# Performance work log

Hardware: AMD Instinct MI355X
Metric: run time of the kernel (lower is better)

## Reference

```python
import jax, jax.numpy as jnp
import numpy as np

B, T, I, H, L = 32, 1024, 1024, 1024, 3


def setup_inputs() -> dict:
    key = jax.random.key(0)
    ks = jax.random.split(key, 8)
    sc_in = 1.0 / np.sqrt(I)
    sc_h = 1.0 / np.sqrt(H)
    return {
        "x": jax.random.normal(ks[0], (B, T, I), dtype=jnp.float32),
        "s0": jnp.zeros((B, H), dtype=jnp.float32),
        "w_h": jax.random.normal(ks[1], (I, H), dtype=jnp.float32) * sc_in,
        "w_t": jax.random.normal(ks[2], (I, H), dtype=jnp.float32) * sc_in,
        "w_c": jax.random.normal(ks[3], (I, H), dtype=jnp.float32) * sc_in,
        "Rh": jax.random.normal(ks[4], (L, H, H), dtype=jnp.float32) * sc_h,
        "Rt": jax.random.normal(ks[5], (L, H, H), dtype=jnp.float32) * sc_h,
        "Rc": jax.random.normal(ks[6], (L, H, H), dtype=jnp.float32) * sc_h,
        "bh": jnp.zeros((L, H), dtype=jnp.float32),
        "bt": jnp.zeros((L, H), dtype=jnp.float32),
        "bc": jnp.zeros((L, H), dtype=jnp.float32),
    }


def reference(x, s0, w_h, w_t, w_c, Rh, Rt, Rc, bh, bt, bc):
    # x: [B, T, I]; s0: [B, H]. Dropout prob = 0 -> identity.
    num_layers = Rh.shape[0]

    def step(s, x_t):
        # Input projections only feed layer 0 (as in the torch code).
        whx = x_t @ w_h  # [B, H]
        wtx = x_t @ w_t
        wcx = x_t @ w_c
        for l in range(num_layers):
            h_in = (whx if l == 0 else 0.0) + s @ Rh[l].T + bh[l]
            t_in = (wtx if l == 0 else 0.0) + s @ Rt[l].T + bt[l]
            c_in = (wcx if l == 0 else 0.0) + s @ Rc[l].T + bc[l]
            h = jnp.tanh(h_in)
            t = jax.nn.sigmoid(t_in)
            c = jax.nn.sigmoid(c_in)
            s = h * t + s * c
        return s, s

    x_tbi = jnp.swapaxes(x, 0, 1)  # [T, B, I] for scan over time
    s_T, outs = jax.lax.scan(step, s0, x_tbi)
    return jnp.swapaxes(outs, 0, 1), s_T  # ([B, T, H], [B, H])
```

## Files before the change

### kernel.cpp

```cpp
#include <hip/hip_runtime.h>
#include <hip/hip_bf16.h>

static constexpr int Bb = 32;
static constexpr int Tt = 1024;
static constexpr int Ii = 1024;
static constexpr int Hh = 1024;
static constexpr int NWG = 256;

static constexpr int HSLOT = Hh * 16;
static constexpr int NSLOT2 = 2 * (3 * Tt + 1);

typedef float f4 __attribute__((ext_vector_type(4)));

static constexpr int LDS_WORDS = 36 * 1024 + 4 * 12 * 16;
static constexpr int LDS_BYTES = LDS_WORDS * 4;

static constexpr int SYNC_BYTES = 4096;

template <typename PT> __device__ __forceinline__ float pt_to_f(PT v);
template <> __device__ __forceinline__ float pt_to_f<float>(float v) { return v; }
template <> __device__ __forceinline__ float pt_to_f<__hip_bfloat16>(__hip_bfloat16 v) { return __bfloat162float(v); }

template <typename PT> __device__ __forceinline__ PT f_to_pt(float v);
template <> __device__ __forceinline__ float f_to_pt<float>(float v) { return v; }
template <> __device__ __forceinline__ __hip_bfloat16 f_to_pt<__hip_bfloat16>(float v) { return __float2bfloat16(v); }

#define CGLD(dst, p, lit) \
    asm volatile("global_load_dwordx4 %0, %1, off offset:" lit : "=v"(dst) : "v"(p))
#define GB4(sv, p, a,b,c,d2) \
    CGLD(sv[0],p,a); CGLD(sv[1],p,b); CGLD(sv[2],p,c); CGLD(sv[3],p,d2)
#define VWAIT(n) do { asm volatile("s_waitcnt vmcnt(" #n ")" ::: "memory"); \
                      __builtin_amdgcn_sched_barrier(0); } while (0)

template <typename PT>
__global__ __launch_bounds__(256, 2) void proj_gemm(
    const float* __restrict__ X, const float* __restrict__ Wh,
    const float* __restrict__ Wt, const float* __restrict__ Wc,
    PT* __restrict__ P2)
{
    __shared__ float smem[4160];
    float* As = smem;
    float* Bs = smem + 1088;

    const int tid = threadIdx.x;
    const int tx = tid & 15, ty = tid >> 4;
    const int col0 = blockIdx.x * 64;
    const int t0 = blockIdx.y * 2;

    float acc[3][4][4];
#pragma unroll
    for (int g = 0; g < 3; ++g)
#pragma unroll
        for (int mm = 0; mm < 4; ++mm)
#pragma unroll
            for (int nn = 0; nn < 4; ++nn) acc[g][mm][nn] = 0.f;

    const int lm = tid >> 2, lk4 = (tid & 3) * 4;
    const float* aptr = X + ((size_t)(lm & 31) * Tt + (t0 + (lm >> 5))) * Ii + lk4;
    const int bk = tid >> 4, bn4 = (tid & 15) * 4;

    for (int k0 = 0; k0 < Ii; k0 += 16) {
        float4 av = *(const float4*)(aptr + k0);
        As[(lk4 + 0) * 68 + lm] = av.x;
        As[(lk4 + 1) * 68 + lm] = av.y;
        As[(lk4 + 2) * 68 + lm] = av.z;
        As[(lk4 + 3) * 68 + lm] = av.w;
        *(float4*)&Bs[0 * 1024 + bk * 64 + bn4] = *(const float4*)(Wh + (size_t)(k0 + bk) * Hh + col0 + bn4);
        *(float4*)&Bs[1 * 1024 + bk * 64 + bn4] = *(const float4*)(Wt + (size_t)(k0 + bk) * Hh + col0 + bn4);
        *(float4*)&Bs[2 * 1024 + bk * 64 + bn4] = *(const float4*)(Wc + (size_t)(k0 + bk) * Hh + col0 + bn4);
        __syncthreads();
#pragma unroll
        for (int k = 0; k < 16; ++k) {
            float4 a = *(const float4*)&As[k * 68 + ty * 4];
            float a_[4] = {a.x, a.y, a.z, a.w};
#pragma unroll
            for (int g = 0; g < 3; ++g) {
                float4 b = *(const float4*)&Bs[g * 1024 + k * 64 + tx * 4];
                float b_[4] = {b.x, b.y, b.z, b.w};
#pragma unroll
                for (int mm = 0; mm < 4; ++mm)
#pragma unroll
                    for (int nn = 0; nn < 4; ++nn)
                        acc[g][mm][nn] += a_[mm] * b_[nn];
            }
        }
        __syncthreads();
    }

    float* E = smem;
    const int b4 = (tid & 7) * 4;
#pragma unroll 1
    for (int g = 0; g < 3; ++g) {
        __syncthreads();
#pragma unroll
        for (int mm = 0; mm < 4; ++mm)
#pragma unroll
            for (int nn = 0; nn < 4; ++nn)
                E[(ty * 4 + mm) * 65 + tx * 4 + nn] = acc[g][mm][nn];
        __syncthreads();
        PT* dst = P2 + (size_t)g * Tt * Hh * Bb;
#pragma unroll
        for (int it = 0; it < 4; ++it) {
            const int line = (tid >> 3) + it * 32;
            const int tt = line >> 6, hh = line & 63;
            const float o0 = E[(tt * 32 + b4 + 0) * 65 + hh];
            const float o1 = E[(tt * 32 + b4 + 1) * 65 + hh];
            const float o2v = E[(tt * 32 + b4 + 2) * 65 + hh];
            const float o3 = E[(tt * 32 + b4 + 3) * 65 + hh];
            PT* d = dst + ((size_t)(t0 + tt) * Hh + col0 + hh) * Bb + b4;
            d[0] = f_to_pt<PT>(o0); d[1] = f_to_pt<PT>(o1);
            d[2] = f_to_pt<PT>(o2v); d[3] = f_to_pt<PT>(o3);
        }
    }
}

template <typename RT>
__global__ void init_k(const float* __restrict__ s0, RT* __restrict__ ring)
{
    const int i = blockIdx.x * 256 + threadIdx.x;
    if (i < Bb * Hh) {
        const int b = i >> 10, h = i & 1023;
        const int grp = b >> 4, bl = b & 15;
        ring[(size_t)grp * HSLOT + h * 16 + bl] = f_to_pt<RT>(s0[i]);
    }
}

template <typename RT>
__global__ __launch_bounds__(256) void out_transpose(
    const RT* __restrict__ ring, float* __restrict__ out, float* __restrict__ sT)
{
    __shared__ float tile[128 * 33];
    const int tid = threadIdx.x;
    const int h0 = blockIdx.x * 128;
    const int t = blockIdx.y;
    const RT* srcA = ring + (size_t)((3 * t + 3) * 2) * HSLOT + h0 * 16;
    const RT* srcB = srcA + HSLOT;
#pragma unroll
    for (int e = 0; e < 16; ++e) {
        const int idx = e * 256 + tid;
        const int h = idx >> 5, b = idx & 31;
        const float v = (b < 16) ? pt_to_f<RT>(srcA[h * 16 + b])
                                 : pt_to_f<RT>(srcB[h * 16 + (b - 16)]);
        tile[h * 33 + b] = v;
    }
    __syncthreads();
    const int hi = tid & 31, bq = tid >> 5;
#pragma unroll
    for (int e = 0; e < 4; ++e) {
        const int b = bq + e * 8;
        float4 v;
        v.x = tile[(hi * 4 + 0) * 33 + b];
        v.y = tile[(hi * 4 + 1) * 33 + b];
        v.z = tile[(hi * 4 + 2) * 33 + b];
        v.w = tile[(hi * 4 + 3) * 33 + b];
        *(float4*)(out + ((size_t)b * Tt + t) * Hh + h0 + hi * 4) = v;
        if (t == Tt - 1) *(float4*)(sT + (size_t)b * Hh + h0 + hi * 4) = v;
    }
}

__device__ __forceinline__ void poll256(unsigned* flags, int tid, unsigned ph)
{
    if (tid < 64) {
        for (;;) {
            const unsigned v0 = __hip_atomic_load(&flags[tid],       __ATOMIC_RELAXED, __HIP_MEMORY_SCOPE_AGENT);
            const unsigned v1 = __hip_atomic_load(&flags[tid + 64],  __ATOMIC_RELAXED, __HIP_MEMORY_SCOPE_AGENT);
            const unsigned v2 = __hip_atomic_load(&flags[tid + 128], __ATOMIC_RELAXED, __HIP_MEMORY_SCOPE_AGENT);
            const unsigned v3 = __hip_atomic_load(&flags[tid + 192], __ATOMIC_RELAXED, __HIP_MEMORY_SCOPE_AGENT);
            if (__all((int)((v0 >= ph) & (v1 >= ph) & (v2 >= ph) & (v3 >= ph)))) break;
            __builtin_amdgcn_s_sleep(2);
        }
    }
    __syncthreads();
}

template <typename PT, typename RT>
__global__ __launch_bounds__(256, 1) void rhn_recur(
    const float* __restrict__ Rh, const float* __restrict__ Rt,
    const float* __restrict__ Rc, const float* __restrict__ bh,
    const float* __restrict__ bt, const float* __restrict__ bc,
    const PT* __restrict__ P2, RT* __restrict__ ring,
    unsigned* __restrict__ flagsA, unsigned* __restrict__ flagsB)
{
    extern __shared__ float lds[];
    float* part = lds + 36 * 1024;

    const int g = blockIdx.x;
    const int tid = threadIdx.x;

    {
        const int k4 = tid * 4;
        const int sk = k4 ^ (((k4 >> 5) & 3) << 2);
#pragma unroll 1
        for (int j = 0; j < 36; ++j) {
            const int l = j / 12;
            const int rem = j - l * 12;
            const int gt = rem >> 2;
            const int q = rem & 3;
            const int h = (q << 8) | g;
            const float* src = (gt == 0 ? Rh : (gt == 1 ? Rt : Rc)) + ((size_t)l * Hh + h) * Hh;
            *(float4*)&lds[(j << 10) | sk] = *(const float4*)(src + k4);
        }
    }
    __syncthreads();

    const int ks = tid >> 2;
    const int bq = tid & 3;
    const int b0 = bq << 2;
    const int wv = tid >> 6;
    const int jsel = ks & 15;
    const int ubb = tid & 15;
    const int uq  = (tid >> 4) & 3;
    const int uhc = (uq << 8) | g;

    int o2[4];
#pragma unroll
    for (int c = 0; c < 4; ++c)
        o2[c] = (((ks << 4) | (c << 2))) ^ ((((ks << 4) >> 5) & 3) << 2);

    float brh[3], brt[3], brc[3];
#pragma unroll
    for (int l = 0; l < 3; ++l) {
        brh[l] = bh[l * Hh + uhc];
        brt[l] = bt[l * Hh + uhc];
        brc[l] = bc[l * Hh + uhc];
    }

    float soA = pt_to_f<RT>(ring[uhc * 16 + ubb]);
    float soB = pt_to_f<RT>(ring[(size_t)HSLOT + uhc * 16 + ubb]);

    const size_t THB = (size_t)Tt * Hh * Bb;
    float pvA0 = 0.f, pvA1 = 0.f, pvA2 = 0.f, pvB0 = 0.f, pvB1 = 0.f, pvB2 = 0.f;
    auto loadP = [&](int tt) {
        if (tid < 64) {
            const size_t pb = ((size_t)tt * Hh + uhc) * Bb + ubb;
            pvA0 = pt_to_f<PT>(P2[pb]);
            pvA1 = pt_to_f<PT>(P2[THB + pb]);
            pvA2 = pt_to_f<PT>(P2[2 * THB + pb]);
            pvB0 = pt_to_f<PT>(P2[pb + 16]);
            pvB1 = pt_to_f<PT>(P2[THB + pb + 16]);
            pvB2 = pt_to_f<PT>(P2[2 * THB + pb + 16]);
        }
    };
    loadP(0);

    auto halfstep = [&](const float* rp, const RT* rs, RT* rw, float& so,
                        float pv0, float pv1, float pv2, bool addP,
                        float bb0, float bb1, float bb2) {
        f4 accv[12];
#pragma unroll
        for (int jj = 0; jj < 12; ++jj) accv[jj] = (f4){0.f, 0.f, 0.f, 0.f};

        if constexpr (sizeof(RT) == 4) {
            const float* sA = (const float*)rs + (size_t)(ks << 4) * 16 + b0;
            f4 sv0[4], sv1[4], sv2[4], sv3[4];
            GB4(sv0, sA, "0","64","128","192");
            GB4(sv1, sA, "256","320","384","448");
            GB4(sv2, sA, "512","576","640","704");
            GB4(sv3, sA, "768","832","896","960");
            VWAIT(12);
#pragma unroll
            for (int jj = 0; jj < 12; ++jj) {
                const f4 r = *(const f4*)(rp + jj * 1024 + o2[0]);
                f4 a = accv[jj];
                a += sv0[0] * r[0]; a += sv0[1] * r[1]; a += sv0[2] * r[2]; a += sv0[3] * r[3];
                accv[jj] = a;
            }
            VWAIT(8);
#pragma unroll
            for (int jj = 0; jj < 12; ++jj) {
                const f4 r = *(const f4*)(rp + jj * 1024 + o2[1]);
                f4 a = accv[jj];
                a += sv1[0] * r[0]; a += sv1[1] * r[1]; a += sv1[2] * r[2]; a += sv1[3] * r[3];
                accv[jj] = a;
            }
            VWAIT(4);
#pragma unroll
            for (int jj = 0; jj < 12; ++jj) {
                const f4 r = *(const f4*)(rp + jj * 1024 + o2[2]);
                f4 a = accv[jj];
                a += sv2[0] * r[0]; a += sv2[1] * r[1]; a += sv2[2] * r[2]; a += sv2[3] * r[3];
                accv[jj] = a;
            }
            VWAIT(0);
#pragma unroll
            for (int jj = 0; jj < 12; ++jj) {
                const f4 r = *(const f4*)(rp + jj * 1024 + o2[3]);
                f4 a = accv[jj];
                a += sv3[0] * r[0]; a += sv3[1] * r[1]; a += sv3[2] * r[2]; a += sv3[3] * r[3];
                accv[jj] = a;
            }
        } else {
            const __hip_bfloat16* sIn = (const __hip_bfloat16*)rs + (size_t)(ks << 4) * 16 + b0;
#pragma unroll
            for (int blk = 0; blk < 4; ++blk) {
                f4 sv[4];
#pragma unroll
                for (int i = 0; i < 4; ++i) {
                    const ushort4 u = *(const ushort4*)(sIn + (size_t)(blk * 4 + i) * 16);
                    sv[i][0] = __uint_as_float((unsigned)u.x << 16);
                    sv[i][1] = __uint_as_float((unsigned)u.y << 16);
                    sv[i][2] = __uint_as_float((unsigned)u.z << 16);
                    sv[i][3] = __uint_as_float((unsigned)u.w << 16);
                }
#pragma unroll
                for (int jj = 0; jj < 12; ++jj) {
                    const f4 r = *(const f4*)(rp + jj * 1024 + o2[blk]);
                    f4 a = accv[jj];
                    a += sv[0] * r[0]; a += sv[1] * r[1]; a += sv[2] * r[2]; a += sv[3] * r[3];
                    accv[jj] = a;
                }
            }
        }

#pragma unroll
        for (int jj = 0; jj < 12; ++jj) {
#pragma unroll
            for (int st = 4; st <= 32; st <<= 1) {
                accv[jj][0] += __shfl_xor(accv[jj][0], st);
                accv[jj][1] += __shfl_xor(accv[jj][1], st);
                accv[jj][2] += __shfl_xor(accv[jj][2], st);
                accv[jj][3] += __shfl_xor(accv[jj][3], st);
            }
        }
        f4 s1 = accv[0];
#pragma unroll
        for (int j2 = 1; j2 < 12; ++j2) if (jsel == j2) s1 = accv[j2];
        if (jsel < 12) *(f4*)&part[wv * 192 + jsel * 16 + b0] = s1;
        __syncthreads();

        if (tid < 64) {
            float vals[3];
#pragma unroll
            for (int gt = 0; gt < 3; ++gt) {
                const int jl = (gt << 2) + uq;
                vals[gt] = part[jl * 16 + ubb] + part[192 + jl * 16 + ubb]
                         + part[384 + jl * 16 + ubb] + part[576 + jl * 16 + ubb];
            }
            vals[0] += bb0; vals[1] += bb1; vals[2] += bb2;
            if (addP) { vals[0] += pv0; vals[1] += pv1; vals[2] += pv2; }
            const float hv = 1.f - 2.f / (1.f + __expf(2.f * vals[0]));
            const float tv = 1.f / (1.f + __expf(-vals[1]));
            const float cv = 1.f / (1.f + __expf(-vals[2]));
            const float sn = hv * tv + so * cv;
            so = sn;
            RT* wp = rw + uhc * 16 + ubb;
            if constexpr (sizeof(RT) == 4) {
                __hip_atomic_store((float*)wp, sn, __ATOMIC_RELAXED, __HIP_MEMORY_SCOPE_AGENT);
            } else {
                __hip_bfloat16 b16 = __float2bfloat16(sn);
                __hip_atomic_store((unsigned short*)wp, *(unsigned short*)&b16,
                                   __ATOMIC_RELAXED, __HIP_MEMORY_SCOPE_AGENT);
            }
        }
        __syncthreads();
    };

#pragma unroll 1
    for (int t = 0; t < Tt; ++t) {
#pragma unroll 1
        for (int l = 0; l < 3; ++l) {
            const int p = t * 3 + l;
            float bb0, bb1, bb2;
            if (l == 0)      { bb0 = brh[0]; bb1 = brt[0]; bb2 = brc[0]; }
            else if (l == 1) { bb0 = brh[1]; bb1 = brt[1]; bb2 = brc[1]; }
            else             { bb0 = brh[2]; bb1 = brt[2]; bb2 = brc[2]; }
            const float* rp = lds + l * 12288;

            poll256(flagsA, tid, (unsigned)p);
            halfstep(rp, ring + (size_t)(p * 2 + 0) * HSLOT,
                         ring + (size_t)((p + 1) * 2 + 0) * HSLOT,
                     soA, pvA0, pvA1, pvA2, l == 0, bb0, bb1, bb2);
            if (tid == 0)
                __hip_atomic_store(&flagsA[g], (unsigned)(p + 1), __ATOMIC_RELAXED, __HIP_MEMORY_SCOPE_AGENT);

            poll256(flagsB, tid, (unsigned)p);
            halfstep(rp, ring + (size_t)(p * 2 + 1) * HSLOT,
                         ring + (size_t)((p + 1) * 2 + 1) * HSLOT,
                     soB, pvB0, pvB1, pvB2, l == 0, bb0, bb1, bb2);
            if (tid == 0)
                __hip_atomic_store(&flagsB[g], (unsigned)(p + 1), __ATOMIC_RELAXED, __HIP_MEMORY_SCOPE_AGENT);

            if (l == 2 && t + 1 < Tt) loadP(t + 1);
        }
    }
}

extern "C" void kernel_launch(void* const* d_in, const int* in_sizes, int n_in,
                              void* d_out, int out_size, void* d_ws, size_t ws_size,
                              hipStream_t stream)
{
    (void)in_sizes; (void)n_in; (void)out_size;
    const float* x  = (const float*)d_in[0];
    const float* s0 = (const float*)d_in[1];
    const float* wh = (const float*)d_in[2];
    const float* wt = (const float*)d_in[3];
    const float* wc = (const float*)d_in[4];
    const float* Rh = (const float*)d_in[5];
    const float* Rt = (const float*)d_in[6];
    const float* Rc = (const float*)d_in[7];
    const float* bh = (const float*)d_in[8];
    const float* bt = (const float*)d_in[9];
    const float* bc = (const float*)d_in[10];

    float* out = (float*)d_out;
    float* sT  = out + (size_t)Bb * Tt * Hh;

    const size_t THB  = (size_t)Tt * Hh * Bb;
    const size_t p2f  = 3 * THB * 4, p2h = 3 * THB * 2;
    const size_t ringF = (size_t)NSLOT2 * HSLOT * 4;
    const size_t ringH = (size_t)NSLOT2 * HSLOT * 2;

    char* w = (char*)d_ws;

    if (ws_size >= p2f + ringF + SYNC_BYTES) {
        float* P2 = (float*)w;
        float* ring = (float*)(w + p2f);
        unsigned* flagsA = (unsigned*)(w + p2f + ringF);
        unsigned* flagsB = flagsA + 256;
        hipMemsetAsync(flagsA, 0, SYNC_BYTES, stream);
        proj_gemm<float><<<dim3(16, 512), 256, 0, stream>>>(x, wh, wt, wc, P2);
        init_k<float><<<128, 256, 0, stream>>>(s0, ring);
        hipFuncSetAttribute(reinterpret_cast<const void*>(rhn_recur<float, float>),
                            hipFuncAttributeMaxDynamicSharedMemorySize, LDS_BYTES);
        void* args[] = {(void*)&Rh, (void*)&Rt, (void*)&Rc, (void*)&bh, (void*)&bt, (void*)&bc,
                        (void*)&P2, (void*)&ring, (void*)&flagsA, (void*)&flagsB};
        hipLaunchCooperativeKernel(reinterpret_cast<void*>(rhn_recur<float, float>),
                                   dim3(NWG), dim3(256), args, LDS_BYTES, stream);
        out_transpose<float><<<dim3(8, 1024), 256, 0, stream>>>(ring, out, sT);
    } else if (ws_size >= p2h + ringF + SYNC_BYTES) {
        __hip_bfloat16* P2 = (__hip_bfloat16*)w;
        float* ring = (float*)(w + p2h);
        unsigned* flagsA = (unsigned*)(w + p2h + ringF);
        unsigned* flagsB = flagsA + 256;
        hipMemsetAsync(flagsA, 0, SYNC_BYTES, stream);
        proj_gemm<__hip_bfloat16><<<dim3(16, 512), 256, 0, stream>>>(x, wh, wt, wc, P2);
        init_k<float><<<128, 256, 0, stream>>>(s0, ring);
        hipFuncSetAttribute(reinterpret_cast<const void*>(rhn_recur<__hip_bfloat16, float>),
                            hipFuncAttributeMaxDynamicSharedMemorySize, LDS_BYTES);
        void* args[] = {(void*)&Rh, (void*)&Rt, (void*)&Rc, (void*)&bh, (void*)&bt, (void*)&bc,
                        (void*)&P2, (void*)&ring, (void*)&flagsA, (void*)&flagsB};
        hipLaunchCooperativeKernel(reinterpret_cast<void*>(rhn_recur<__hip_bfloat16, float>),
                                   dim3(NWG), dim3(256), args, LDS_BYTES, stream);
        out_transpose<float><<<dim3(8, 1024), 256, 0, stream>>>(ring, out, sT);
    } else {
        __hip_bfloat16* P2 = (__hip_bfloat16*)w;
        __hip_bfloat16* ring = (__hip_bfloat16*)(w + p2h);
        unsigned* flagsA = (unsigned*)(w + p2h + ringH);
        unsigned* flagsB = flagsA + 256;
        hipMemsetAsync(flagsA, 0, SYNC_BYTES, stream);
        proj_gemm<__hip_bfloat16><<<dim3(16, 512), 256, 0, stream>>>(x, wh, wt, wc, P2);
        init_k<__hip_bfloat16><<<128, 256, 0, stream>>>(s0, ring);
        hipFuncSetAttribute(reinterpret_cast<const void*>(rhn_recur<__hip_bfloat16, __hip_bfloat16>),
                            hipFuncAttributeMaxDynamicSharedMemorySize, LDS_BYTES);
        void* args[] = {(void*)&Rh, (void*)&Rt, (void*)&Rc, (void*)&bh, (void*)&bt, (void*)&bc,
                        (void*)&P2, (void*)&ring, (void*)&flagsA, (void*)&flagsB};
        hipLaunchCooperativeKernel(reinterpret_cast<void*>(rhn_recur<__hip_bfloat16, __hip_bfloat16>),
                                   dim3(NWG), dim3(256), args, LDS_BYTES, stream);
        out_transpose<__hip_bfloat16><<<dim3(8, 1024), 256, 0, stream>>>(ring, out, sT);
    }
}
```

Measured before the change: 33.34 ms.

## Replace flag-based grid barriers with sentinel-poisoned ring data polling

Removes the per-half-step flag arrays and all-workgroup polling barriers. The state ring is pre-filled with a NaN sentinel pattern, and consumers spin on the actual data loads (retrying with cache-bypassing loads) until no sentinel values remain. The per-halfstep syncthreads goes away by double-buffering the LDS partial-sum area, and the next-timestep P prefetch is moved earlier. This trades a full grid-wide barrier for fine-grained dataflow waiting, at the cost of a larger init kernel that writes the whole ring and reliance on stores becoming visible atomically per element.

```diff
diff --git a/kernel.cpp b/kernel.cpp
--- a/kernel.cpp
+++ b/kernel.cpp
@@ -12,10 +12,11 @@
 
 typedef float f4 __attribute__((ext_vector_type(4)));
 
-static constexpr int LDS_WORDS = 36 * 1024 + 4 * 12 * 16;
+static constexpr int LDS_WORDS = 36 * 1024 + 2 * 768;
 static constexpr int LDS_BYTES = LDS_WORDS * 4;
 
-static constexpr int SYNC_BYTES = 4096;
+static constexpr unsigned SENT32 = 0x7FC0DEADu;
+static constexpr unsigned SENT16 = 0x7FC1u;
 
 template <typename PT> __device__ __forceinline__ float pt_to_f(PT v);
 template <> __device__ __forceinline__ float pt_to_f<float>(float v) { return v; }
@@ -27,10 +28,48 @@
 
 #define CGLD(dst, p, lit) \
     asm volatile("global_load_dwordx4 %0, %1, off offset:" lit : "=v"(dst) : "v"(p))
-#define GB4(sv, p, a,b,c,d2) \
+#define CG4(sv, p, a,b,c,d2) \
     CGLD(sv[0],p,a); CGLD(sv[1],p,b); CGLD(sv[2],p,c); CGLD(sv[3],p,d2)
+#define BGLD(dst, p, lit) \
+    asm volatile("global_load_dwordx4 %0, %1, off offset:" lit " sc0 sc1" : "=v"(dst) : "v"(p))
+#define BG4(sv, p, a,b,c,d2) \
+    BGLD(sv[0],p,a); BGLD(sv[1],p,b); BGLD(sv[2],p,c); BGLD(sv[3],p,d2)
+#define CGLD2(dst, p, lit) \
+    asm volatile("global_load_dwordx2 %0, %1, off offset:" lit : "=v"(dst) : "v"(p))
+#define CG4x2(su, p, a,b,c,d2) \
+    CGLD2(su[0],p,a); CGLD2(su[1],p,b); CGLD2(su[2],p,c); CGLD2(su[3],p,d2)
+#define BGLD2(dst, p, lit) \
+    asm volatile("global_load_dwordx2 %0, %1, off offset:" lit " sc0 sc1" : "=v"(dst) : "v"(p))
+#define BG4x2(su, p, a,b,c,d2) \
+    BGLD2(su[0],p,a); BGLD2(su[1],p,b); BGLD2(su[2],p,c); BGLD2(su[3],p,d2)
 #define VWAIT(n) do { asm volatile("s_waitcnt vmcnt(" #n ")" ::: "memory"); \
                       __builtin_amdgcn_sched_barrier(0); } while (0)
+
+__device__ __forceinline__ int grp4_ok32(const f4* sv) {
+    int ok = 1;
+#pragma unroll
+    for (int i = 0; i < 4; ++i)
+#pragma unroll
+        for (int j = 0; j < 4; ++j)
+            ok &= (__float_as_uint(sv[i][j]) != SENT32);
+    return ok;
+}
+__device__ __forceinline__ int grp4_ok16(const uint2* su) {
+    int ok = 1;
+#pragma unroll
+    for (int i = 0; i < 4; ++i) {
+        ok &= ((su[i].x & 0xFFFFu) != SENT16) & ((su[i].x >> 16) != SENT16);
+        ok &= ((su[i].y & 0xFFFFu) != SENT16) & ((su[i].y >> 16) != SENT16);
+    }
+    return ok;
+}
+#define RETRY4(sv, p, a,b,c,d2) \
+    { int _tr = 0; \
+      while (!__all(grp4_ok32(sv))) { \
+          if (_tr++) __builtin_amdgcn_s_sleep(2); \
+          BG4(sv, p, a,b,c,d2); \
+          VWAIT(0); \
+      } }
 
 template <typename PT>
 __global__ __launch_bounds__(256, 2) void proj_gemm(
@@ -115,14 +154,21 @@
 }
 
 template <typename RT>
-__global__ void init_k(const float* __restrict__ s0, RT* __restrict__ ring)
+__global__ __launch_bounds__(256) void init_ring(const float* __restrict__ s0,
+                                                 RT* __restrict__ ring)
 {
-    const int i = blockIdx.x * 256 + threadIdx.x;
-    if (i < Bb * Hh) {
-        const int b = i >> 10, h = i & 1023;
+    const size_t tid = (size_t)blockIdx.x * 256 + threadIdx.x;
+    if (tid < (size_t)Bb * Hh) {
+        const int b = (int)(tid >> 10), h = (int)(tid & 1023);
         const int grp = b >> 4, bl = b & 15;
-        ring[(size_t)grp * HSLOT + h * 16 + bl] = f_to_pt<RT>(s0[i]);
-    }
+        ring[(size_t)grp * HSLOT + h * 16 + bl] = f_to_pt<RT>(s0[tid]);
+    }
+    const unsigned sw = (sizeof(RT) == 4) ? SENT32 : ((SENT16 << 16) | SENT16);
+    const uint4 pat = {sw, sw, sw, sw};
+    uint4* base = (uint4*)(ring + 2 * (size_t)HSLOT);
+    const size_t n16 = (size_t)(NSLOT2 - 2) * HSLOT * sizeof(RT) / 16;
+    const size_t stride = (size_t)gridDim.x * 256;
+    for (size_t i = tid; i < n16; i += stride) base[i] = pat;
 }
 
 template <typename RT>
@@ -158,31 +204,16 @@
     }
 }
 
-__device__ __forceinline__ void poll256(unsigned* flags, int tid, unsigned ph)
-{
-    if (tid < 64) {
-        for (;;) {
-            const unsigned v0 = __hip_atomic_load(&flags[tid],       __ATOMIC_RELAXED, __HIP_MEMORY_SCOPE_AGENT);
-            const unsigned v1 = __hip_atomic_load(&flags[tid + 64],  __ATOMIC_RELAXED, __HIP_MEMORY_SCOPE_AGENT);
-            const unsigned v2 = __hip_atomic_load(&flags[tid + 128], __ATOMIC_RELAXED, __HIP_MEMORY_SCOPE_AGENT);
-            const unsigned v3 = __hip_atomic_load(&flags[tid + 192], __ATOMIC_RELAXED, __HIP_MEMORY_SCOPE_AGENT);
-            if (__all((int)((v0 >= ph) & (v1 >= ph) & (v2 >= ph) & (v3 >= ph)))) break;
-            __builtin_amdgcn_s_sleep(2);
-        }
-    }
-    __syncthreads();
-}
-
 template <typename PT, typename RT>
 __global__ __launch_bounds__(256, 1) void rhn_recur(
     const float* __restrict__ Rh, const float* __restrict__ Rt,
     const float* __restrict__ Rc, const float* __restrict__ bh,
     const float* __restrict__ bt, const float* __restrict__ bc,
-    const PT* __restrict__ P2, RT* __restrict__ ring,
-    unsigned* __restrict__ flagsA, unsigned* __restrict__ flagsB)
+    const PT* __restrict__ P2, RT* __restrict__ ring)
 {
     extern __shared__ float lds[];
-    float* part = lds + 36 * 1024;
+    float* partA = lds + 36 * 1024;
+    float* partB = partA + 768;
 
     const int g = blockIdx.x;
     const int tid = threadIdx.x;
@@ -245,7 +276,7 @@
 
     auto halfstep = [&](const float* rp, const RT* rs, RT* rw, float& so,
                         float pv0, float pv1, float pv2, bool addP,
-                        float bb0, float bb1, float bb2) {
+                        float bb0, float bb1, float bb2, float* part) {
         f4 accv[12];
 #pragma unroll
         for (int jj = 0; jj < 12; ++jj) accv[jj] = (f4){0.f, 0.f, 0.f, 0.f};
@@ -253,11 +284,12 @@
         if constexpr (sizeof(RT) == 4) {
             const float* sA = (const float*)rs + (size_t)(ks << 4) * 16 + b0;
             f4 sv0[4], sv1[4], sv2[4], sv3[4];
-            GB4(sv0, sA, "0","64","128","192");
-            GB4(sv1, sA, "256","320","384","448");
-            GB4(sv2, sA, "512","576","640","704");
-            GB4(sv3, sA, "768","832","896","960");
+            CG4(sv0, sA, "0","64","128","192");
+            CG4(sv1, sA, "256","320","384","448");
+            CG4(sv2, sA, "512","576","640","704");
+            CG4(sv3, sA, "768","832","896","960");
             VWAIT(12);
+            RETRY4(sv0, sA, "0","64","128","192");
 #pragma unroll
             for (int jj = 0; jj < 12; ++jj) {
                 const f4 r = *(const f4*)(rp + jj * 1024 + o2[0]);
@@ -266,6 +298,7 @@
                 accv[jj] = a;
             }
             VWAIT(8);
+            RETRY4(sv1, sA, "256","320","384","448");
 #pragma unroll
             for (int jj = 0; jj < 12; ++jj) {
                 const f4 r = *(const f4*)(rp + jj * 1024 + o2[1]);
@@ -274,6 +307,7 @@
                 accv[jj] = a;
             }
             VWAIT(4);
+            RETRY4(sv2, sA, "512","576","640","704");
 #pragma unroll
             for (int jj = 0; jj < 12; ++jj) {
                 const f4 r = *(const f4*)(rp + jj * 1024 + o2[2]);
@@ -282,6 +316,7 @@
                 accv[jj] = a;
             }
             VWAIT(0);
+            RETRY4(sv3, sA, "768","832","896","960");
 #pragma unroll
             for (int jj = 0; jj < 12; ++jj) {
                 const f4 r = *(const f4*)(rp + jj * 1024 + o2[3]);
@@ -291,16 +326,25 @@
             }
         } else {
             const __hip_bfloat16* sIn = (const __hip_bfloat16*)rs + (size_t)(ks << 4) * 16 + b0;
-#pragma unroll
+#pragma unroll 1
             for (int blk = 0; blk < 4; ++blk) {
+                uint2 su[4];
+                const __hip_bfloat16* pb2 = sIn + (size_t)blk * 64;
+                CG4x2(su, pb2, "0","32","64","96");
+                VWAIT(0);
+                int _tr = 0;
+                while (!__all(grp4_ok16(su))) {
+                    if (_tr++) __builtin_amdgcn_s_sleep(2);
+                    BG4x2(su, pb2, "0","32","64","96");
+                    VWAIT(0);
+                }
                 f4 sv[4];
 #pragma unroll
                 for (int i = 0; i < 4; ++i) {
-                    const ushort4 u = *(const ushort4*)(sIn + (size_t)(blk * 4 + i) * 16);
-                    sv[i][0] = __uint_as_float((unsigned)u.x << 16);
-                    sv[i][1] = __uint_as_float((unsigned)u.y << 16);
-                    sv[i][2] = __uint_as_float((unsigned)u.z << 16);
-                    sv[i][3] = __uint_as_float((unsigned)u.w << 16);
+                    sv[i][0] = __uint_as_float(su[i].x << 16);
+                    sv[i][1] = __uint_as_float(su[i].x & 0xFFFF0000u);
+                    sv[i][2] = __uint_as_float(su[i].y << 16);
+                    sv[i][3] = __uint_as_float(su[i].y & 0xFFFF0000u);
                 }
 #pragma unroll
                 for (int jj = 0; jj < 12; ++jj) {
@@ -352,7 +396,6 @@
                                    __ATOMIC_RELAXED, __HIP_MEMORY_SCOPE_AGENT);
             }
         }
-        __syncthreads();
     };
 
 #pragma unroll 1
@@ -366,21 +409,14 @@
             else             { bb0 = brh[2]; bb1 = brt[2]; bb2 = brc[2]; }
             const float* rp = lds + l * 12288;
 
-            poll256(flagsA, tid, (unsigned)p);
             halfstep(rp, ring + (size_t)(p * 2 + 0) * HSLOT,
                          ring + (size_t)((p + 1) * 2 + 0) * HSLOT,
-                     soA, pvA0, pvA1, pvA2, l == 0, bb0, bb1, bb2);
-            if (tid == 0)
-                __hip_atomic_store(&flagsA[g], (unsigned)(p + 1), __ATOMIC_RELAXED, __HIP_MEMORY_SCOPE_AGENT);
-
-            poll256(flagsB, tid, (unsigned)p);
+                     soA, pvA0, pvA1, pvA2, l == 0, bb0, bb1, bb2, partA);
             halfstep(rp, ring + (size_t)(p * 2 + 1) * HSLOT,
                          ring + (size_t)((p + 1) * 2 + 1) * HSLOT,
-                     soB, pvB0, pvB1, pvB2, l == 0, bb0, bb1, bb2);
-            if (tid == 0)
-                __hip_atomic_store(&flagsB[g], (unsigned)(p + 1), __ATOMIC_RELAXED, __HIP_MEMORY_SCOPE_AGENT);
-
-            if (l == 2 && t + 1 < Tt) loadP(t + 1);
+                     soB, pvB0, pvB1, pvB2, l == 0, bb0, bb1, bb2, partB);
+
+            if (l == 1 && t + 1 < Tt) loadP(t + 1);
         }
     }
 }
@@ -412,48 +448,39 @@
 
     char* w = (char*)d_ws;
 
-    if (ws_size >= p2f + ringF + SYNC_BYTES) {
+    if (ws_size >= p2f + ringF) {
         float* P2 = (float*)w;
         float* ring = (float*)(w + p2f);
-        unsigned* flagsA = (unsigned*)(w + p2f + ringF);
-        unsigned* flagsB = flagsA + 256;
-        hipMemsetAsync(flagsA, 0, SYNC_BYTES, stream);
         proj_gemm<float><<<dim3(16, 512), 256, 0, stream>>>(x, wh, wt, wc, P2);
-        init_k<float><<<128, 256, 0, stream>>>(s0, ring);
+        init_ring<float><<<2048, 256, 0, stream>>>(s0, ring);
         hipFuncSetAttribute(reinterpret_cast<const void*>(rhn_recur<float, float>),
                             hipFuncAttributeMaxDynamicSharedMemorySize, LDS_BYTES);
         void* args[] = {(void*)&Rh, (void*)&Rt, (void*)&Rc, (void*)&bh, (void*)&bt, (void*)&bc,
-                        (void*)&P2, (void*)&ring, (void*)&flagsA, (void*)&flagsB};
+                        (void*)&P2, (void*)&ring};
         hipLaunchCooperativeKernel(reinterpret_cast<void*>(rhn_recur<float, float>),
                                    dim3(NWG), dim3(256), args, LDS_BYTES, stream);
         out_transpose<float><<<dim3(8, 1024), 256, 0, stream>>>(ring, out, sT);
-    } else if (ws_size >= p2h + ringF + SYNC_BYTES) {
+    } else if (ws_size >= p2h + ringF) {
         __hip_bfloat16* P2 = (__hip_bfloat16*)w;
         float* ring = (float*)(w + p2h);
-        unsigned* flagsA = (unsigned*)(w + p2h + ringF);
-        unsigned* flagsB = flagsA + 256;
-        hipMemsetAsync(flagsA, 0, SYNC_BYTES, stream);
         proj_gemm<__hip_bfloat16><<<dim3(16, 512), 256, 0, stream>>>(x, wh, wt, wc, P2);
-        init_k<float><<<128, 256, 0, stream>>>(s0, ring);
+        init_ring<float><<<2048, 256, 0, stream>>>(s0, ring);
         hipFuncSetAttribute(reinterpret_cast<const void*>(rhn_recur<__hip_bfloat16, float>),
                             hipFuncAttributeMaxDynamicSharedMemorySize, LDS_BYTES);
         void* args[] = {(void*)&Rh, (void*)&Rt, (void*)&Rc, (void*)&bh, (void*)&bt, (void*)&bc,
-                        (void*)&P2, (void*)&ring, (void*)&flagsA, (void*)&flagsB};
+                        (void*)&P2, (void*)&ring};
         hipLaunchCooperativeKernel(reinterpret_cast<void*>(rhn_recur<__hip_bfloat16, float>),
                                    dim3(NWG), dim3(256), args, LDS_BYTES, stream);
         out_transpose<float><<<dim3(8, 1024), 256, 0, stream>>>(ring, out, sT);
     } else {
         __hip_bfloat16* P2 = (__hip_bfloat16*)w;
         __hip_bfloat16* ring = (__hip_bfloat16*)(w + p2h);
-        unsigned* flagsA = (unsigned*)(w + p2h + ringH);
-        unsigned* flagsB = flagsA + 256;
-        hipMemsetAsync(flagsA, 0, SYNC_BYTES, stream);
         proj_gemm<__hip_bfloat16><<<dim3(16, 512), 256, 0, stream>>>(x, wh, wt, wc, P2);
-        init_k<__hip_bfloat16><<<128, 256, 0, stream>>>(s0, ring);
+        init_ring<__hip_bfloat16><<<2048, 256, 0, stream>>>(s0, ring);
         hipFuncSetAttribute(reinterpret_cast<const void*>(rhn_recur<__hip_bfloat16, __hip_bfloat16>),
                             hipFuncAttributeMaxDynamicSharedMemorySize, LDS_BYTES);
         void* args[] = {(void*)&Rh, (void*)&Rt, (void*)&Rc, (void*)&bh, (void*)&bt, (void*)&bc,
-                        (void*)&P2, (void*)&ring, (void*)&flagsA, (void*)&flagsB};
+                        (void*)&P2, (void*)&ring};
         hipLaunchCooperativeKernel(reinterpret_cast<void*>(rhn_recur<__hip_bfloat16, __hip_bfloat16>),
                                    dim3(NWG), dim3(256), args, LDS_BYTES, stream);
         out_transpose<__hip_bfloat16><<<dim3(8, 1024), 256, 0, stream>>>(ring, out, sT);
```

New measurement: 39.41 ms. +18.2%, slower.
